# Kernel optimization log

Hardware: AMD Instinct MI355X
Metric: run time of the kernel (lower is better)

Reference implementation:

```python
import jax, jax.numpy as jnp
import numpy as np

NUM_EXPERTS = 8
TOP_K = 2

def setup_inputs() -> dict:
    key = jax.random.key(0)
    ks = jax.random.split(key, 5)
    B, S, H, I, E = 4, 2048, 1024, 2816, NUM_EXPERTS
    return {
        "hidden_states": jax.random.normal(ks[0], (B, S, H), dtype=jnp.float32),
        "gate_w": jax.random.normal(ks[1], (H, E), dtype=jnp.float32) / np.sqrt(H),
        "w_gate": jax.random.normal(ks[2], (E, H, I), dtype=jnp.float32) / np.sqrt(H),
        "w_up": jax.random.normal(ks[3], (E, H, I), dtype=jnp.float32) / np.sqrt(H),
        "w_down": jax.random.normal(ks[4], (E, I, H), dtype=jnp.float32) / np.sqrt(I),
    }

def reference(hidden_states, gate_w, w_gate, w_up, w_down):
    B, S, H = hidden_states.shape
    x = hidden_states.reshape(-1, H)                      # [T, H]
    router_logits = x @ gate_w                            # [T, E]
    probs = jax.nn.softmax(router_logits.astype(jnp.float32), axis=-1)
    topk_w, sel = jax.lax.top_k(probs, TOP_K)             # [T, K]
    topk_w = topk_w / jnp.sum(topk_w, axis=-1, keepdims=True)
    topk_w = topk_w.astype(x.dtype)
    out = jnp.zeros_like(x)
    for e in range(NUM_EXPERTS):
        # combine weight for this expert per token (0 if not routed)
        we = jnp.sum(jnp.where(sel == e, topk_w, 0.0), axis=-1)  # [T]
        h = jax.nn.silu(x @ w_gate[e]) * (x @ w_up[e])           # [T, I]
        out = out + (h @ w_down[e]) * we[:, None]
    return out.reshape(B, S, H), router_logits
```

## Files before the change

### kernel.cpp

```cpp
#include <hip/hip_runtime.h>
#include <hip/hip_bf16.h>
#include <stdint.h>

typedef unsigned short u16;
typedef unsigned int u32;

#define T_TOK 8192
#define H_DIM 1024
#define I_DIM 2816
#define NE 8

typedef __bf16 bf16x8 __attribute__((ext_vector_type(8)));
typedef float f32x4 __attribute__((ext_vector_type(4)));

union F8 { uint4 v; bf16x8 f; u32 w[4]; };

__device__ __forceinline__ u16 f2bf(float f) {
    u32 u = __float_as_uint(f);
    u32 r = u + 0x7FFFu + ((u >> 16) & 1u);
    return (u16)(r >> 16);
}
__device__ __forceinline__ u32 pkbf(float a, float b) {
    float2 f; f.x = a; f.y = b;
    __hip_bfloat162 h = __float22bfloat162_rn(f);
    union { __hip_bfloat162 h2; u32 w; } cv; cv.h2 = h;
    return cv.w;
}

__device__ __forceinline__ void g2l16(const void* g, void* l) {
    __builtin_amdgcn_global_load_lds(
        (const __attribute__((address_space(1))) u32*)g,
        (__attribute__((address_space(3))) u32*)l, 16, 0, 0);
}

__global__ void zero_cnt_kernel(int* __restrict__ cnt) {
    if (threadIdx.x < NE) cnt[threadIdx.x] = 0;
}

__global__ void __launch_bounds__(256) zero_out_kernel(float* __restrict__ out0) {
    int gid = blockIdx.x * 256 + threadIdx.x;
    f32x4 z = {0.f, 0.f, 0.f, 0.f};
    ((f32x4*)out0)[gid] = z;
}

__global__ void __launch_bounds__(256) xcvt_kernel(const float* __restrict__ x, u16* __restrict__ xb) {
    size_t gid = (size_t)blockIdx.x * 256 + threadIdx.x;
    const float4* s = (const float4*)x + gid * 2;
    float4 a = s[0], b = s[1];
    uint4 o;
    o.x = pkbf(a.x, a.y); o.y = pkbf(a.z, a.w);
    o.z = pkbf(b.x, b.y); o.w = pkbf(b.z, b.w);
    ((uint4*)xb)[gid] = o;
}

__global__ void __launch_bounds__(256)
pack_kernel(const float* __restrict__ src, u32* __restrict__ dst, int K, int N) {
    int e = blockIdx.z;
    int n0 = blockIdx.x * 64;
    int r0 = blockIdx.y * 128;
    __shared__ float sT[128][65];
    int tid = threadIdx.x;
    const float* sp = src + ((size_t)e * K + r0) * N + n0;
#pragma unroll
    for (int rep = 0; rep < 8; rep++) {
        int row = rep * 16 + (tid >> 4);
        int n4 = (tid & 15) * 4;
        float4 v = *(const float4*)(sp + (size_t)row * N + n4);
        sT[row][n4] = v.x; sT[row][n4 + 1] = v.y; sT[row][n4 + 2] = v.z; sT[row][n4 + 3] = v.w;
    }
    __syncthreads();
    int n = tid >> 2, q = tid & 3;
    u32* dp = dst + ((size_t)e * N + n0 + n) * (size_t)(K >> 1) + (r0 >> 1) + q * 16;
    uint4 o[4];
    u32* ow = (u32*)o;
#pragma unroll
    for (int j = 0; j < 16; j++) {
        int k2 = q * 16 + j;
        ow[j] = pkbf(sT[2 * k2][n], sT[2 * k2 + 1][n]);
    }
#pragma unroll
    for (int j = 0; j < 4; j++) ((uint4*)dp)[j] = o[j];
}

__global__ void __launch_bounds__(256)
router_kernel(const float* __restrict__ x, const float* __restrict__ gw,
              float* __restrict__ logits_out, float* __restrict__ wbuf,
              int* __restrict__ cnt, int* __restrict__ idxlist) {
    int lane = threadIdx.x & 63;
    int t = blockIdx.x * 4 + (threadIdx.x >> 6);
    const float* xr = x + (size_t)t * H_DIM;
    float acc[NE];
#pragma unroll
    for (int e = 0; e < NE; e++) acc[e] = 0.f;
#pragma unroll
    for (int i = 0; i < 16; i++) {
        int hh = i * 64 + lane;
        float xv = xr[hh];
        const float4* grow = (const float4*)(gw + (size_t)hh * NE);
        float4 g0 = grow[0], g1 = grow[1];
        acc[0] += xv * g0.x; acc[1] += xv * g0.y;
        acc[2] += xv * g0.z; acc[3] += xv * g0.w;
        acc[4] += xv * g1.x; acc[5] += xv * g1.y;
        acc[6] += xv * g1.z; acc[7] += xv * g1.w;
    }
#pragma unroll
    for (int m = 32; m >= 1; m >>= 1) {
#pragma unroll
        for (int e = 0; e < NE; e++) acc[e] += __shfl_xor(acc[e], m, 64);
    }
    if (lane == 0) {
        float mx = acc[0];
#pragma unroll
        for (int e = 1; e < NE; e++) mx = fmaxf(mx, acc[e]);
        float p[NE];
#pragma unroll
        for (int e = 0; e < NE; e++) p[e] = __expf(acc[e] - mx);
        float4 l0, l1;
        l0.x = acc[0]; l0.y = acc[1]; l0.z = acc[2]; l0.w = acc[3];
        l1.x = acc[4]; l1.y = acc[5]; l1.z = acc[6]; l1.w = acc[7];
        float4* lrow_p = (float4*)(logits_out + (size_t)t * NE);
        lrow_p[0] = l0; lrow_p[1] = l1;
        int a = 0; float pa = p[0];
#pragma unroll
        for (int e = 1; e < NE; e++) if (p[e] > pa) { a = e; pa = p[e]; }
        int b = -1; float pb = -1.f;
#pragma unroll
        for (int e = 0; e < NE; e++) if (e != a && p[e] > pb) { b = e; pb = p[e]; }
        if (b < 0) { b = a ^ 1; pb = p[b]; }
        float inv = 1.f / (pa + pb);
        wbuf[2 * t]     = pa * inv;
        wbuf[2 * t + 1] = pb * inv;
        int pos = atomicAdd(&cnt[a], 1); idxlist[a * T_TOK + pos] = 2 * t;
        pos = atomicAdd(&cnt[b], 1);     idxlist[b * T_TOK + pos] = 2 * t + 1;
    }
}

__global__ void __launch_bounds__(256)
gateup_kernel(const u16* __restrict__ xb, const u32* __restrict__ wgp,
              const u32* __restrict__ wup, const int* __restrict__ cnt,
              const int* __restrict__ idxlist, u16* __restrict__ hchunk,
              int nbase, int nlen) {
    int NN = nlen >> 7;
    int pid = blockIdx.x;
    int xcd = pid & 7;
    int j = pid >> 3;
    int m = j & 63;
    int gs = j >> 6;
    int g = xcd + (gs << 3);
    int e = g / NN;
    int nb = g - e * NN;
    int c = cnt[e];
    int m0 = m * 128;
    if (m0 >= c) return;
    int n0l = nb * 128;
    int n0g = nbase + n0l;

    __shared__ alignas(16) u16 sA[128 * 64];
    __shared__ alignas(16) u32 sBg[128 * 32];
    __shared__ alignas(16) u32 sBu[128 * 32];
    int tid = threadIdx.x;
    int wv = tid >> 6;

    int arow = tid >> 3;
    int cswz = tid & 7;
    const u16* aP[4];
#pragma unroll
    for (int p = 0; p < 4; p++) {
        int row = p * 32 + arow;
        int jj = m0 + row; if (jj > c - 1) jj = c - 1;
        int slot = idxlist[e * T_TOK + jj];
        aP[p] = xb + (size_t)(slot >> 1) * H_DIM + ((cswz ^ (row & 7)) << 3);
    }
    size_t bn = (size_t)e * I_DIM + n0g + arow;
    int bsw = (cswz ^ (arow & 7)) << 2;
    const u32* bgB = wgp + bn * 512 + bsw;
    const u32* buB = wup + bn * 512 + bsw;

    int lane = tid & 63;
    int wm = (tid >> 7) & 1, wn = (tid >> 6) & 1;
    int lrow = lane & 15, quad = lane >> 4;
    f32x4 zero = {0.f, 0.f, 0.f, 0.f};
    f32x4 accg[4][4], accu[4][4];
#pragma unroll
    for (int mi = 0; mi < 4; mi++)
#pragma unroll
        for (int ni = 0; ni < 4; ni++) { accg[mi][ni] = zero; accu[mi][ni] = zero; }

    for (int k0 = 0; k0 < H_DIM; k0 += 64) {
        __syncthreads();
#pragma unroll
        for (int p = 0; p < 4; p++)
            g2l16(aP[p] + k0, sA + (size_t)(p * 256 + wv * 64) * 8);
#pragma unroll
        for (int p = 0; p < 4; p++)
            g2l16(bgB + (size_t)p * 32 * 512 + (k0 >> 1), sBg + (size_t)(p * 256 + wv * 64) * 4);
#pragma unroll
        for (int p = 0; p < 4; p++)
            g2l16(buB + (size_t)p * 32 * 512 + (k0 >> 1), sBu + (size_t)(p * 256 + wv * 64) * 4);
        __syncthreads();
#pragma unroll
        for (int kk = 0; kk < 2; kk++) {
            int cb = kk * 4 + quad;
            bf16x8 af[4]; F8 bg[4], bu[4];
#pragma unroll
            for (int i = 0; i < 4; i++) {
                int ra = wm * 64 + i * 16 + lrow;
                af[i] = *(const bf16x8*)(sA + (size_t)(ra * 8 + (cb ^ (ra & 7))) * 8);
                int n = wn * 64 + i * 16 + lrow;
                bg[i].v = *(const uint4*)(sBg + (size_t)(n * 8 + (cb ^ (n & 7))) * 4);
                bu[i].v = *(const uint4*)(sBu + (size_t)(n * 8 + (cb ^ (n & 7))) * 4);
            }
#pragma unroll
            for (int mi = 0; mi < 4; mi++)
#pragma unroll
                for (int ni = 0; ni < 4; ni++) {
                    accg[mi][ni] = __builtin_amdgcn_mfma_f32_16x16x32_bf16(af[mi], bg[ni].f, accg[mi][ni], 0, 0, 0);
                    accu[mi][ni] = __builtin_amdgcn_mfma_f32_16x16x32_bf16(af[mi], bu[ni].f, accu[mi][ni], 0, 0, 0);
                }
        }
    }
#pragma unroll
    for (int mi = 0; mi < 4; mi++) {
#pragma unroll
        for (int r = 0; r < 4; r++) {
            int grow = m0 + wm * 64 + mi * 16 + quad * 4 + r;
            if (grow < c) {
                int slot = idxlist[e * T_TOK + grow];
                u16* hrow = hchunk + (size_t)slot * nlen + n0l + wn * 64 + lrow;
#pragma unroll
                for (int ni = 0; ni < 4; ni++) {
                    float gv = accg[mi][ni][r], uv = accu[mi][ni][r];
                    float hv = gv * uv / (1.f + __expf(-gv));
                    hrow[ni * 16] = f2bf(hv);
                }
            }
        }
    }
}

__global__ void __launch_bounds__(256)
down_kernel(const u16* __restrict__ hchunk, const u32* __restrict__ wdp,
            const int* __restrict__ cnt, const int* __restrict__ idxlist,
            const float* __restrict__ wbuf, float* __restrict__ out0,
            float* __restrict__ ybuf, int kbase, int klen, int beta) {
    int pid = blockIdx.x;
    int xcd = pid & 7;
    int j = pid >> 3;
    int m = j & 63;
    int gs = j >> 6;
    int g = xcd + (gs << 3);
    int e = g >> 3;
    int nb = g & 7;
    int c = cnt[e];
    int m0 = m * 128;
    if (m0 >= c) return;
    int n0 = nb * 128;

    __shared__ alignas(16) u16 sA[128 * 64];
    __shared__ alignas(16) u32 sB[128 * 32];
    int tid = threadIdx.x;
    int wv = tid >> 6;

    int arow = tid >> 3;
    int cswz = tid & 7;
    const u16* aP[4];
#pragma unroll
    for (int p = 0; p < 4; p++) {
        int row = p * 32 + arow;
        int jj = m0 + row; if (jj > c - 1) jj = c - 1;
        int slot = idxlist[e * T_TOK + jj];
        aP[p] = hchunk + (size_t)slot * klen + ((cswz ^ (row & 7)) << 3);
    }
    int bsw = (cswz ^ (arow & 7)) << 2;
    const u32* bB = wdp + ((size_t)e * H_DIM + n0 + arow) * 1408 + (kbase >> 1) + bsw;

    int lane = tid & 63;
    int wm = (tid >> 7) & 1, wn = (tid >> 6) & 1;
    int lrow = lane & 15, quad = lane >> 4;
    f32x4 zero = {0.f, 0.f, 0.f, 0.f};
    f32x4 acc[4][4];
#pragma unroll
    for (int mi = 0; mi < 4; mi++)
#pragma unroll
        for (int ni = 0; ni < 4; ni++) acc[mi][ni] = zero;

    for (int k0 = 0; k0 < klen; k0 += 64) {
        __syncthreads();
#pragma unroll
        for (int p = 0; p < 4; p++)
            g2l16(aP[p] + k0, sA + (size_t)(p * 256 + wv * 64) * 8);
#pragma unroll
        for (int p = 0; p < 4; p++)
            g2l16(bB + (size_t)p * 32 * 1408 + (k0 >> 1), sB + (size_t)(p * 256 + wv * 64) * 4);
        __syncthreads();
#pragma unroll
        for (int kk = 0; kk < 2; kk++) {
            int cb = kk * 4 + quad;
            bf16x8 af[4]; F8 bf[4];
#pragma unroll
            for (int i = 0; i < 4; i++) {
                int ra = wm * 64 + i * 16 + lrow;
                af[i] = *(const bf16x8*)(sA + (size_t)(ra * 8 + (cb ^ (ra & 7))) * 8);
                int n = wn * 64 + i * 16 + lrow;
                bf[i].v = *(const uint4*)(sB + (size_t)(n * 8 + (cb ^ (n & 7))) * 4);
            }
#pragma unroll
            for (int mi = 0; mi < 4; mi++)
#pragma unroll
                for (int ni = 0; ni < 4; ni++)
                    acc[mi][ni] = __builtin_amdgcn_mfma_f32_16x16x32_bf16(af[mi], bf[ni].f, acc[mi][ni], 0, 0, 0);
        }
    }
#pragma unroll
    for (int mi = 0; mi < 4; mi++) {
#pragma unroll
        for (int r = 0; r < 4; r++) {
            int grow = m0 + wm * 64 + mi * 16 + quad * 4 + r;
            if (grow < c) {
                int slot = idxlist[e * T_TOK + grow];
                if (ybuf) {
                    float* yrow = ybuf + (size_t)slot * H_DIM + n0 + wn * 64 + lrow;
                    if (beta) {
#pragma unroll
                        for (int ni = 0; ni < 4; ni++) yrow[ni * 16] += acc[mi][ni][r];
                    } else {
#pragma unroll
                        for (int ni = 0; ni < 4; ni++) yrow[ni * 16] = acc[mi][ni][r];
                    }
                } else {
                    float w = wbuf[slot];
                    float* yrow = out0 + (size_t)(slot >> 1) * H_DIM + n0 + wn * 64 + lrow;
#pragma unroll
                    for (int ni = 0; ni < 4; ni++)
                        atomicAdd(&yrow[ni * 16], w * acc[mi][ni][r]);
                }
            }
        }
    }
}

__global__ void __launch_bounds__(256)
combine_kernel(const float* __restrict__ ybuf, const float* __restrict__ wbuf,
               float* __restrict__ out0) {
    int gid = blockIdx.x * 256 + threadIdx.x;
    int t = gid >> 8;
    int h4 = gid & 255;
    float w0 = wbuf[2 * t], w1 = wbuf[2 * t + 1];
    f32x4 a = ((const f32x4*)(ybuf + (size_t)(2 * t) * H_DIM))[h4];
    f32x4 b = ((const f32x4*)(ybuf + (size_t)(2 * t + 1) * H_DIM))[h4];
    f32x4 o;
#pragma unroll
    for (int i = 0; i < 4; i++) o[i] = w0 * a[i] + w1 * b[i];
    ((f32x4*)(out0 + (size_t)t * H_DIM))[h4] = o;
}

extern "C" void kernel_launch(void* const* d_in, const int* in_sizes, int n_in,
                              void* d_out, int out_size, void* d_ws, size_t ws_size,
                              hipStream_t stream) {
    (void)in_sizes; (void)n_in; (void)out_size;
    const float* x  = (const float*)d_in[0];
    const float* gw = (const float*)d_in[1];
    const float* wg = (const float*)d_in[2];
    const float* wu = (const float*)d_in[3];
    const float* wd = (const float*)d_in[4];
    float* out = (float*)d_out;
    float* logits = out + (size_t)T_TOK * H_DIM;
    char* ws = (char*)d_ws;

    size_t off = 0;
    auto take = [&](size_t sz) { char* p = ws + off; off += (sz + 255) & ~(size_t)255; return p; };
    int* cnt      = (int*)take(NE * 4);
    int* idxlist  = (int*)take((size_t)NE * T_TOK * 4);
    float* wbuf   = (float*)take((size_t)2 * T_TOK * 4);
    u16* xb       = (u16*)take((size_t)T_TOK * H_DIM * 2);
    u32* wgp      = (u32*)take((size_t)NE * I_DIM * 512 * 4);
    u32* wup      = (u32*)take((size_t)NE * I_DIM * 512 * 4);
    u32* wdp      = (u32*)take((size_t)NE * H_DIM * 1408 * 4);
    float* ybuf = nullptr;
    size_t ybytes = (size_t)2 * T_TOK * H_DIM * 4;
    size_t minh   = (size_t)2 * T_TOK * 128 * 2 + 256;
    if (ws_size >= off + ybytes + minh) ybuf = (float*)take(ybytes);
    int ich = I_DIM;
    while (ich > 128 && off + (size_t)2 * T_TOK * ich * 2 > ws_size) ich -= 128;
    u16* hchunk = (u16*)(ws + off);

    zero_cnt_kernel<<<1, 64, 0, stream>>>(cnt);
    if (!ybuf) zero_out_kernel<<<T_TOK * H_DIM / 4 / 256, 256, 0, stream>>>(out);
    pack_kernel<<<dim3(I_DIM / 64, H_DIM / 128, NE), 256, 0, stream>>>(wg, wgp, H_DIM, I_DIM);
    pack_kernel<<<dim3(I_DIM / 64, H_DIM / 128, NE), 256, 0, stream>>>(wu, wup, H_DIM, I_DIM);
    pack_kernel<<<dim3(H_DIM / 64, I_DIM / 128, NE), 256, 0, stream>>>(wd, wdp, I_DIM, H_DIM);
    xcvt_kernel<<<T_TOK * H_DIM / 8 / 256, 256, 0, stream>>>(x, xb);
    router_kernel<<<T_TOK / 4, 256, 0, stream>>>(x, gw, logits, wbuf, cnt, idxlist);
    for (int base = 0; base < I_DIM; base += ich) {
        int len = I_DIM - base; if (len > ich) len = ich;
        int NN = len / 128;
        gateup_kernel<<<64 * NN * NE, 256, 0, stream>>>(xb, wgp, wup, cnt, idxlist, hchunk, base, len);
        down_kernel<<<64 * 8 * NE, 256, 0, stream>>>(hchunk, wdp, cnt, idxlist, wbuf, out, ybuf, base, len, base > 0 ? 1 : 0);
    }
    if (ybuf) combine_kernel<<<T_TOK * H_DIM / 4 / 256, 256, 0, stream>>>(ybuf, wbuf, out);
}
```

Baseline: 1.158 ms.

## Double-buffer LDS tiles with K=32 steps in gate/up and down GEMMs

Both expert GEMM kernels change from a single 64-wide K tile, loaded between two barriers, to two 32-wide LDS buffers. The next tile is prefetched while MFMAs run on the current one, with one barrier per step. The XOR swizzle is reworked for four 16-byte chunks per row, and launch bounds now request 3 blocks per CU. The goal is to hide global-to-LDS load latency behind compute. In exchange there are twice as many barrier steps, and the narrower swizzle and register cap may cause bank conflicts or spills.

After: 1.349 ms. 16.5% more time.

```diff
diff --git a/kernel.cpp b/kernel.cpp
--- a/kernel.cpp
+++ b/kernel.cpp
@@ -135,7 +135,7 @@
     }
 }
 
-__global__ void __launch_bounds__(256)
+__global__ void __launch_bounds__(256, 3)
 gateup_kernel(const u16* __restrict__ xb, const u32* __restrict__ wgp,
               const u32* __restrict__ wup, const int* __restrict__ cnt,
               const int* __restrict__ idxlist, u16* __restrict__ hchunk,
@@ -155,26 +155,38 @@
     int n0l = nb * 128;
     int n0g = nbase + n0l;
 
-    __shared__ alignas(16) u16 sA[128 * 64];
-    __shared__ alignas(16) u32 sBg[128 * 32];
-    __shared__ alignas(16) u32 sBu[128 * 32];
+    __shared__ alignas(16) u16 sA[2][128 * 32];
+    __shared__ alignas(16) u32 sBg[2][128 * 16];
+    __shared__ alignas(16) u32 sBu[2][128 * 16];
     int tid = threadIdx.x;
     int wv = tid >> 6;
 
-    int arow = tid >> 3;
-    int cswz = tid & 7;
-    const u16* aP[4];
-#pragma unroll
-    for (int p = 0; p < 4; p++) {
-        int row = p * 32 + arow;
+    int row_lo = tid >> 2;
+    int csw = tid & 3;
+    const u16* aP[2];
+#pragma unroll
+    for (int p = 0; p < 2; p++) {
+        int row = p * 64 + row_lo;
         int jj = m0 + row; if (jj > c - 1) jj = c - 1;
         int slot = idxlist[e * T_TOK + jj];
-        aP[p] = xb + (size_t)(slot >> 1) * H_DIM + ((cswz ^ (row & 7)) << 3);
-    }
-    size_t bn = (size_t)e * I_DIM + n0g + arow;
-    int bsw = (cswz ^ (arow & 7)) << 2;
+        aP[p] = xb + (size_t)(slot >> 1) * H_DIM + ((csw ^ (row_lo & 3)) << 3);
+    }
+    size_t bn = (size_t)e * I_DIM + n0g + row_lo;
+    int bsw = (csw ^ (row_lo & 3)) << 2;
     const u32* bgB = wgp + bn * 512 + bsw;
     const u32* buB = wup + bn * 512 + bsw;
+
+    auto stage = [&](int k0, int buf) {
+#pragma unroll
+        for (int p = 0; p < 2; p++)
+            g2l16(aP[p] + k0, &sA[buf][(p * 256 + wv * 64) * 8]);
+#pragma unroll
+        for (int p = 0; p < 2; p++)
+            g2l16(bgB + (size_t)p * 64 * 512 + (k0 >> 1), &sBg[buf][(p * 256 + wv * 64) * 4]);
+#pragma unroll
+        for (int p = 0; p < 2; p++)
+            g2l16(buB + (size_t)p * 64 * 512 + (k0 >> 1), &sBu[buf][(p * 256 + wv * 64) * 4]);
+    };
 
     int lane = tid & 63;
     int wm = (tid >> 7) & 1, wn = (tid >> 6) & 1;
@@ -186,38 +198,28 @@
 #pragma unroll
         for (int ni = 0; ni < 4; ni++) { accg[mi][ni] = zero; accu[mi][ni] = zero; }
 
-    for (int k0 = 0; k0 < H_DIM; k0 += 64) {
+    stage(0, 0);
+#pragma unroll 2
+    for (int k0 = 0; k0 < H_DIM; k0 += 32) {
+        int buf = (k0 >> 5) & 1;
         __syncthreads();
-#pragma unroll
-        for (int p = 0; p < 4; p++)
-            g2l16(aP[p] + k0, sA + (size_t)(p * 256 + wv * 64) * 8);
-#pragma unroll
-        for (int p = 0; p < 4; p++)
-            g2l16(bgB + (size_t)p * 32 * 512 + (k0 >> 1), sBg + (size_t)(p * 256 + wv * 64) * 4);
-#pragma unroll
-        for (int p = 0; p < 4; p++)
-            g2l16(buB + (size_t)p * 32 * 512 + (k0 >> 1), sBu + (size_t)(p * 256 + wv * 64) * 4);
-        __syncthreads();
-#pragma unroll
-        for (int kk = 0; kk < 2; kk++) {
-            int cb = kk * 4 + quad;
-            bf16x8 af[4]; F8 bg[4], bu[4];
-#pragma unroll
-            for (int i = 0; i < 4; i++) {
-                int ra = wm * 64 + i * 16 + lrow;
-                af[i] = *(const bf16x8*)(sA + (size_t)(ra * 8 + (cb ^ (ra & 7))) * 8);
-                int n = wn * 64 + i * 16 + lrow;
-                bg[i].v = *(const uint4*)(sBg + (size_t)(n * 8 + (cb ^ (n & 7))) * 4);
-                bu[i].v = *(const uint4*)(sBu + (size_t)(n * 8 + (cb ^ (n & 7))) * 4);
+        if (k0 + 32 < H_DIM) stage(k0 + 32, buf ^ 1);
+        bf16x8 af[4]; F8 bg[4], bu[4];
+#pragma unroll
+        for (int i = 0; i < 4; i++) {
+            int ra = wm * 64 + i * 16 + lrow;
+            af[i] = *(const bf16x8*)&sA[buf][((ra << 2) + (quad ^ (ra & 3))) * 8];
+            int n = wn * 64 + i * 16 + lrow;
+            bg[i].v = *(const uint4*)&sBg[buf][((n << 2) + (quad ^ (n & 3))) * 4];
+            bu[i].v = *(const uint4*)&sBu[buf][((n << 2) + (quad ^ (n & 3))) * 4];
+        }
+#pragma unroll
+        for (int mi = 0; mi < 4; mi++)
+#pragma unroll
+            for (int ni = 0; ni < 4; ni++) {
+                accg[mi][ni] = __builtin_amdgcn_mfma_f32_16x16x32_bf16(af[mi], bg[ni].f, accg[mi][ni], 0, 0, 0);
+                accu[mi][ni] = __builtin_amdgcn_mfma_f32_16x16x32_bf16(af[mi], bu[ni].f, accu[mi][ni], 0, 0, 0);
             }
-#pragma unroll
-            for (int mi = 0; mi < 4; mi++)
-#pragma unroll
-                for (int ni = 0; ni < 4; ni++) {
-                    accg[mi][ni] = __builtin_amdgcn_mfma_f32_16x16x32_bf16(af[mi], bg[ni].f, accg[mi][ni], 0, 0, 0);
-                    accu[mi][ni] = __builtin_amdgcn_mfma_f32_16x16x32_bf16(af[mi], bu[ni].f, accu[mi][ni], 0, 0, 0);
-                }
-        }
     }
 #pragma unroll
     for (int mi = 0; mi < 4; mi++) {
@@ -238,7 +240,7 @@
     }
 }
 
-__global__ void __launch_bounds__(256)
+__global__ void __launch_bounds__(256, 3)
 down_kernel(const u16* __restrict__ hchunk, const u32* __restrict__ wdp,
             const int* __restrict__ cnt, const int* __restrict__ idxlist,
             const float* __restrict__ wbuf, float* __restrict__ out0,
@@ -256,23 +258,32 @@
     if (m0 >= c) return;
     int n0 = nb * 128;
 
-    __shared__ alignas(16) u16 sA[128 * 64];
-    __shared__ alignas(16) u32 sB[128 * 32];
+    __shared__ alignas(16) u16 sA[2][128 * 32];
+    __shared__ alignas(16) u32 sB[2][128 * 16];
     int tid = threadIdx.x;
     int wv = tid >> 6;
 
-    int arow = tid >> 3;
-    int cswz = tid & 7;
-    const u16* aP[4];
-#pragma unroll
-    for (int p = 0; p < 4; p++) {
-        int row = p * 32 + arow;
+    int row_lo = tid >> 2;
+    int csw = tid & 3;
+    const u16* aP[2];
+#pragma unroll
+    for (int p = 0; p < 2; p++) {
+        int row = p * 64 + row_lo;
         int jj = m0 + row; if (jj > c - 1) jj = c - 1;
         int slot = idxlist[e * T_TOK + jj];
-        aP[p] = hchunk + (size_t)slot * klen + ((cswz ^ (row & 7)) << 3);
-    }
-    int bsw = (cswz ^ (arow & 7)) << 2;
-    const u32* bB = wdp + ((size_t)e * H_DIM + n0 + arow) * 1408 + (kbase >> 1) + bsw;
+        aP[p] = hchunk + (size_t)slot * klen + ((csw ^ (row_lo & 3)) << 3);
+    }
+    int bsw = (csw ^ (row_lo & 3)) << 2;
+    const u32* bB = wdp + ((size_t)e * H_DIM + n0 + row_lo) * 1408 + (kbase >> 1) + bsw;
+
+    auto stage = [&](int k0, int buf) {
+#pragma unroll
+        for (int p = 0; p < 2; p++)
+            g2l16(aP[p] + k0, &sA[buf][(p * 256 + wv * 64) * 8]);
+#pragma unroll
+        for (int p = 0; p < 2; p++)
+            g2l16(bB + (size_t)p * 64 * 1408 + (k0 >> 1), &sB[buf][(p * 256 + wv * 64) * 4]);
+    };
 
     int lane = tid & 63;
     int wm = (tid >> 7) & 1, wn = (tid >> 6) & 1;
@@ -284,32 +295,25 @@
 #pragma unroll
         for (int ni = 0; ni < 4; ni++) acc[mi][ni] = zero;
 
-    for (int k0 = 0; k0 < klen; k0 += 64) {
+    stage(0, 0);
+#pragma unroll 2
+    for (int k0 = 0; k0 < klen; k0 += 32) {
+        int buf = (k0 >> 5) & 1;
         __syncthreads();
-#pragma unroll
-        for (int p = 0; p < 4; p++)
-            g2l16(aP[p] + k0, sA + (size_t)(p * 256 + wv * 64) * 8);
-#pragma unroll
-        for (int p = 0; p < 4; p++)
-            g2l16(bB + (size_t)p * 32 * 1408 + (k0 >> 1), sB + (size_t)(p * 256 + wv * 64) * 4);
-        __syncthreads();
-#pragma unroll
-        for (int kk = 0; kk < 2; kk++) {
-            int cb = kk * 4 + quad;
-            bf16x8 af[4]; F8 bf[4];
-#pragma unroll
-            for (int i = 0; i < 4; i++) {
-                int ra = wm * 64 + i * 16 + lrow;
-                af[i] = *(const bf16x8*)(sA + (size_t)(ra * 8 + (cb ^ (ra & 7))) * 8);
-                int n = wn * 64 + i * 16 + lrow;
-                bf[i].v = *(const uint4*)(sB + (size_t)(n * 8 + (cb ^ (n & 7))) * 4);
-            }
-#pragma unroll
-            for (int mi = 0; mi < 4; mi++)
-#pragma unroll
-                for (int ni = 0; ni < 4; ni++)
-                    acc[mi][ni] = __builtin_amdgcn_mfma_f32_16x16x32_bf16(af[mi], bf[ni].f, acc[mi][ni], 0, 0, 0);
+        if (k0 + 32 < klen) stage(k0 + 32, buf ^ 1);
+        bf16x8 af[4]; F8 bf[4];
+#pragma unroll
+        for (int i = 0; i < 4; i++) {
+            int ra = wm * 64 + i * 16 + lrow;
+            af[i] = *(const bf16x8*)&sA[buf][((ra << 2) + (quad ^ (ra & 3))) * 8];
+            int n = wn * 64 + i * 16 + lrow;
+            bf[i].v = *(const uint4*)&sB[buf][((n << 2) + (quad ^ (n & 3))) * 4];
         }
+#pragma unroll
+        for (int mi = 0; mi < 4; mi++)
+#pragma unroll
+            for (int ni = 0; ni < 4; ni++)
+                acc[mi][ni] = __builtin_amdgcn_mfma_f32_16x16x32_bf16(af[mi], bf[ni].f, acc[mi][ni], 0, 0, 0);
     }
 #pragma unroll
     for (int mi = 0; mi < 4; mi++) {
```

## Double-buffer LDS in MoE GEMMs, split gate/up passes, coalesce h stores

Applied to the files above, without the earlier changes.

Both expert GEMM kernels now use two LDS buffers, so the next K-tile's global-to-LDS loads are issued before computing the current tile, with one barrier per iteration instead of two. The gate/up kernel runs the gate and up projections as two sequential passes over one B buffer. The first tile of the up pass is prefetched during the last gate tile. The SiLU*up result is staged through LDS and written as 16-byte row-contiguous stores instead of scattered 2-byte stores. Launch bounds request two blocks per CU. The cost is reloading the gathered activation tile for the second pass, plus extra LDS and register pressure.

Measured after the change: 1.011 ms. 12.7% less time.

```diff
diff --git a/kernel.cpp b/kernel.cpp
--- a/kernel.cpp
+++ b/kernel.cpp
@@ -135,7 +135,7 @@
     }
 }
 
-__global__ void __launch_bounds__(256)
+__global__ void __launch_bounds__(256, 2)
 gateup_kernel(const u16* __restrict__ xb, const u32* __restrict__ wgp,
               const u32* __restrict__ wup, const int* __restrict__ cnt,
               const int* __restrict__ idxlist, u16* __restrict__ hchunk,
@@ -155,26 +155,33 @@
     int n0l = nb * 128;
     int n0g = nbase + n0l;
 
-    __shared__ alignas(16) u16 sA[128 * 64];
-    __shared__ alignas(16) u32 sBg[128 * 32];
-    __shared__ alignas(16) u32 sBu[128 * 32];
+    __shared__ alignas(16) u16 sA[2][128 * 64];
+    __shared__ alignas(16) u32 sB[2][128 * 32];
     int tid = threadIdx.x;
     int wv = tid >> 6;
 
     int arow = tid >> 3;
-    int cswz = tid & 7;
+    int csw = tid & 7;
     const u16* aP[4];
 #pragma unroll
     for (int p = 0; p < 4; p++) {
-        int row = p * 32 + arow;
-        int jj = m0 + row; if (jj > c - 1) jj = c - 1;
+        int jj = m0 + p * 32 + arow; if (jj > c - 1) jj = c - 1;
         int slot = idxlist[e * T_TOK + jj];
-        aP[p] = xb + (size_t)(slot >> 1) * H_DIM + ((cswz ^ (row & 7)) << 3);
+        aP[p] = xb + (size_t)(slot >> 1) * H_DIM + ((csw ^ (arow & 7)) << 3);
     }
     size_t bn = (size_t)e * I_DIM + n0g + arow;
-    int bsw = (cswz ^ (arow & 7)) << 2;
+    int bsw = (csw ^ (arow & 7)) << 2;
     const u32* bgB = wgp + bn * 512 + bsw;
     const u32* buB = wup + bn * 512 + bsw;
+
+    auto stage = [&](int k0, int buf, const u32* bB) {
+#pragma unroll
+        for (int p = 0; p < 4; p++)
+            g2l16(aP[p] + k0, &sA[buf][(p * 256 + wv * 64) * 8]);
+#pragma unroll
+        for (int p = 0; p < 4; p++)
+            g2l16(bB + (size_t)p * 32 * 512 + (k0 >> 1), &sB[buf][(p * 256 + wv * 64) * 4]);
+    };
 
     int lane = tid & 63;
     int wm = (tid >> 7) & 1, wn = (tid >> 6) & 1;
@@ -186,59 +193,72 @@
 #pragma unroll
         for (int ni = 0; ni < 4; ni++) { accg[mi][ni] = zero; accu[mi][ni] = zero; }
 
-    for (int k0 = 0; k0 < H_DIM; k0 += 64) {
-        __syncthreads();
-#pragma unroll
-        for (int p = 0; p < 4; p++)
-            g2l16(aP[p] + k0, sA + (size_t)(p * 256 + wv * 64) * 8);
-#pragma unroll
-        for (int p = 0; p < 4; p++)
-            g2l16(bgB + (size_t)p * 32 * 512 + (k0 >> 1), sBg + (size_t)(p * 256 + wv * 64) * 4);
-#pragma unroll
-        for (int p = 0; p < 4; p++)
-            g2l16(buB + (size_t)p * 32 * 512 + (k0 >> 1), sBu + (size_t)(p * 256 + wv * 64) * 4);
-        __syncthreads();
-#pragma unroll
-        for (int kk = 0; kk < 2; kk++) {
-            int cb = kk * 4 + quad;
-            bf16x8 af[4]; F8 bg[4], bu[4];
-#pragma unroll
-            for (int i = 0; i < 4; i++) {
-                int ra = wm * 64 + i * 16 + lrow;
-                af[i] = *(const bf16x8*)(sA + (size_t)(ra * 8 + (cb ^ (ra & 7))) * 8);
-                int n = wn * 64 + i * 16 + lrow;
-                bg[i].v = *(const uint4*)(sBg + (size_t)(n * 8 + (cb ^ (n & 7))) * 4);
-                bu[i].v = *(const uint4*)(sBu + (size_t)(n * 8 + (cb ^ (n & 7))) * 4);
-            }
-#pragma unroll
-            for (int mi = 0; mi < 4; mi++)
-#pragma unroll
-                for (int ni = 0; ni < 4; ni++) {
-                    accg[mi][ni] = __builtin_amdgcn_mfma_f32_16x16x32_bf16(af[mi], bg[ni].f, accg[mi][ni], 0, 0, 0);
-                    accu[mi][ni] = __builtin_amdgcn_mfma_f32_16x16x32_bf16(af[mi], bu[ni].f, accu[mi][ni], 0, 0, 0);
+    auto run_pass = [&](const u32* bBc, const u32* bBn, f32x4 (&acc)[4][4]) {
+#pragma unroll 2
+        for (int k0 = 0; k0 < H_DIM; k0 += 64) {
+            int buf = (k0 >> 6) & 1;
+            __syncthreads();
+            if (k0 + 64 < H_DIM) stage(k0 + 64, buf ^ 1, bBc);
+            else if (bBn)        stage(0, buf ^ 1, bBn);
+#pragma unroll
+            for (int kk = 0; kk < 2; kk++) {
+                int cb = kk * 4 + quad;
+                bf16x8 af[4]; F8 bf[4];
+#pragma unroll
+                for (int i = 0; i < 4; i++) {
+                    int ra = wm * 64 + i * 16 + lrow;
+                    af[i] = *(const bf16x8*)&sA[buf][(size_t)(ra * 8 + (cb ^ (ra & 7))) * 8];
+                    int n = wn * 64 + i * 16 + lrow;
+                    bf[i].v = *(const uint4*)&sB[buf][(size_t)(n * 8 + (cb ^ (n & 7))) * 4];
                 }
-        }
-    }
-#pragma unroll
-    for (int mi = 0; mi < 4; mi++) {
-#pragma unroll
-        for (int r = 0; r < 4; r++) {
-            int grow = m0 + wm * 64 + mi * 16 + quad * 4 + r;
-            if (grow < c) {
-                int slot = idxlist[e * T_TOK + grow];
-                u16* hrow = hchunk + (size_t)slot * nlen + n0l + wn * 64 + lrow;
-#pragma unroll
-                for (int ni = 0; ni < 4; ni++) {
-                    float gv = accg[mi][ni][r], uv = accu[mi][ni][r];
-                    float hv = gv * uv / (1.f + __expf(-gv));
-                    hrow[ni * 16] = f2bf(hv);
-                }
+#pragma unroll
+                for (int mi = 0; mi < 4; mi++)
+#pragma unroll
+                    for (int ni = 0; ni < 4; ni++)
+                        acc[mi][ni] = __builtin_amdgcn_mfma_f32_16x16x32_bf16(af[mi], bf[ni].f, acc[mi][ni], 0, 0, 0);
             }
         }
-    }
-}
-
-__global__ void __launch_bounds__(256)
+    };
+
+    stage(0, 0, bgB);
+    run_pass(bgB, buB, accg);
+    run_pass(buB, nullptr, accu);
+
+    u16* hT = &sA[0][0];
+    __syncthreads();
+#pragma unroll
+    for (int mi = 0; mi < 4; mi++) {
+#pragma unroll
+        for (int r = 0; r < 4; r++) {
+            int row = wm * 64 + mi * 16 + quad * 4 + r;
+            int swz = (row & 7) << 3;
+#pragma unroll
+            for (int ni = 0; ni < 4; ni++) {
+                int col = wn * 64 + ni * 16 + lrow;
+                float gv = accg[mi][ni][r], uv = accu[mi][ni][r];
+                float hv = gv * uv / (1.f + __expf(-gv));
+                hT[row * 128 + (col ^ swz)] = f2bf(hv);
+            }
+        }
+    }
+    __syncthreads();
+    {
+        int row = tid & 127, half = tid >> 7;
+        int grow = m0 + row;
+        if (grow < c) {
+            int slot = idxlist[e * T_TOK + grow];
+            u16* dst = hchunk + (size_t)slot * nlen + n0l + half * 64;
+            int swz = (row & 7) << 3;
+#pragma unroll
+            for (int j2 = 0; j2 < 8; j2++) {
+                int colb = half * 64 + j2 * 8;
+                *(uint4*)(dst + j2 * 8) = *(const uint4*)&hT[row * 128 + (colb ^ swz)];
+            }
+        }
+    }
+}
+
+__global__ void __launch_bounds__(256, 2)
 down_kernel(const u16* __restrict__ hchunk, const u32* __restrict__ wdp,
             const int* __restrict__ cnt, const int* __restrict__ idxlist,
             const float* __restrict__ wbuf, float* __restrict__ out0,
@@ -256,23 +276,31 @@
     if (m0 >= c) return;
     int n0 = nb * 128;
 
-    __shared__ alignas(16) u16 sA[128 * 64];
-    __shared__ alignas(16) u32 sB[128 * 32];
+    __shared__ alignas(16) u16 sA[2][128 * 64];
+    __shared__ alignas(16) u32 sB[2][128 * 32];
     int tid = threadIdx.x;
     int wv = tid >> 6;
 
     int arow = tid >> 3;
-    int cswz = tid & 7;
+    int csw = tid & 7;
     const u16* aP[4];
 #pragma unroll
     for (int p = 0; p < 4; p++) {
-        int row = p * 32 + arow;
-        int jj = m0 + row; if (jj > c - 1) jj = c - 1;
+        int jj = m0 + p * 32 + arow; if (jj > c - 1) jj = c - 1;
         int slot = idxlist[e * T_TOK + jj];
-        aP[p] = hchunk + (size_t)slot * klen + ((cswz ^ (row & 7)) << 3);
-    }
-    int bsw = (cswz ^ (arow & 7)) << 2;
+        aP[p] = hchunk + (size_t)slot * klen + ((csw ^ (arow & 7)) << 3);
+    }
+    int bsw = (csw ^ (arow & 7)) << 2;
     const u32* bB = wdp + ((size_t)e * H_DIM + n0 + arow) * 1408 + (kbase >> 1) + bsw;
+
+    auto stage = [&](int k0, int buf) {
+#pragma unroll
+        for (int p = 0; p < 4; p++)
+            g2l16(aP[p] + k0, &sA[buf][(p * 256 + wv * 64) * 8]);
+#pragma unroll
+        for (int p = 0; p < 4; p++)
+            g2l16(bB + (size_t)p * 32 * 1408 + (k0 >> 1), &sB[buf][(p * 256 + wv * 64) * 4]);
+    };
 
     int lane = tid & 63;
     int wm = (tid >> 7) & 1, wn = (tid >> 6) & 1;
@@ -284,15 +312,12 @@
 #pragma unroll
         for (int ni = 0; ni < 4; ni++) acc[mi][ni] = zero;
 
+    stage(0, 0);
+#pragma unroll 2
     for (int k0 = 0; k0 < klen; k0 += 64) {
+        int buf = (k0 >> 6) & 1;
         __syncthreads();
-#pragma unroll
-        for (int p = 0; p < 4; p++)
-            g2l16(aP[p] + k0, sA + (size_t)(p * 256 + wv * 64) * 8);
-#pragma unroll
-        for (int p = 0; p < 4; p++)
-            g2l16(bB + (size_t)p * 32 * 1408 + (k0 >> 1), sB + (size_t)(p * 256 + wv * 64) * 4);
-        __syncthreads();
+        if (k0 + 64 < klen) stage(k0 + 64, buf ^ 1);
 #pragma unroll
         for (int kk = 0; kk < 2; kk++) {
             int cb = kk * 4 + quad;
@@ -300,9 +325,9 @@
 #pragma unroll
             for (int i = 0; i < 4; i++) {
                 int ra = wm * 64 + i * 16 + lrow;
-                af[i] = *(const bf16x8*)(sA + (size_t)(ra * 8 + (cb ^ (ra & 7))) * 8);
+                af[i] = *(const bf16x8*)&sA[buf][(size_t)(ra * 8 + (cb ^ (ra & 7))) * 8];
                 int n = wn * 64 + i * 16 + lrow;
-                bf[i].v = *(const uint4*)(sB + (size_t)(n * 8 + (cb ^ (n & 7))) * 4);
+                bf[i].v = *(const uint4*)&sB[buf][(size_t)(n * 8 + (cb ^ (n & 7))) * 4];
             }
 #pragma unroll
             for (int mi = 0; mi < 4; mi++)
```
